# Kernel optimization log

Measured on AMD Instinct MI355X. Metric: run time of the kernel, lower is better.

Reference implementation:

```python
import jax, jax.numpy as jnp
import numpy as np

N_OBJ, N_EVT, N_EDGE, N_MAIN = 50000, 100000, 500000, 25000
OBJ_DIM, EVT_DIM = 256, 256


def setup_inputs() -> dict:
    key = jax.random.key(0)
    ks = jax.random.split(key, 12)
    s = 1.0 / np.sqrt(OBJ_DIM)
    return {
        "object_X": jax.random.normal(ks[0], (N_OBJ, OBJ_DIM), jnp.float32),
        "event_X": jax.random.normal(ks[1], (N_EVT, EVT_DIM), jnp.float32),
        "lc_obj_idx": jax.random.randint(ks[2], (N_EDGE,), 0, N_OBJ),
        "lc_evt_idx": jax.random.randint(ks[3], (N_EDGE,), 0, N_EVT),
        "main_idx": jax.random.randint(ks[4], (N_MAIN,), 0, N_OBJ),
        # lifecycle_proj: Linear(event_dim, obj_dim)
        "W_proj": jax.random.uniform(ks[5], (OBJ_DIM, EVT_DIM), jnp.float32, -s, s),
        "b_proj": jax.random.uniform(ks[6], (OBJ_DIM,), jnp.float32, -s, s),
        # GRUCell(obj_dim, obj_dim): weight_ih/hh are [3*H, H]
        "W_ih": jax.random.uniform(ks[7], (3 * OBJ_DIM, OBJ_DIM), jnp.float32, -s, s),
        "b_ih": jax.random.uniform(ks[8], (3 * OBJ_DIM,), jnp.float32, -s, s),
        "W_hh": jax.random.uniform(ks[9], (3 * OBJ_DIM, OBJ_DIM), jnp.float32, -s, s),
        "b_hh": jax.random.uniform(ks[10], (3 * OBJ_DIM,), jnp.float32, -s, s),
    }


def reference(object_X, event_X, lc_obj_idx, lc_evt_idx, main_idx,
              W_proj, b_proj, W_ih, b_ih, W_hh, b_hh):
    n_obj = object_X.shape[0]
    # gather event feats, linear + ReLU  -> [E, obj_dim]
    proj = jax.nn.relu(event_X[lc_evt_idx] @ W_proj.T + b_proj)
    # scatter_mean over target objects (empty slots -> 0, like torch_scatter)
    sums = jax.ops.segment_sum(proj, lc_obj_idx, num_segments=n_obj)
    cnt = jax.ops.segment_sum(jnp.ones((lc_obj_idx.shape[0],), proj.dtype),
                              lc_obj_idx, num_segments=n_obj)
    profile = sums / jnp.maximum(cnt, 1.0)[:, None]  # [N_obj, obj_dim]
    # GRUCell(profile, object_X)
    gi = profile @ W_ih.T + b_ih   # [N_obj, 3H]
    gh = object_X @ W_hh.T + b_hh  # [N_obj, 3H]
    i_r, i_z, i_n = jnp.split(gi, 3, axis=-1)
    h_r, h_z, h_n = jnp.split(gh, 3, axis=-1)
    r = jax.nn.sigmoid(i_r + h_r)
    z = jax.nn.sigmoid(i_z + h_z)
    n = jnp.tanh(i_n + r * h_n)
    updated = (1.0 - z) * n + z * object_X
    # masked blend: only main objects take updated values
    mask = jnp.zeros((n_obj, 1), object_X.dtype).at[main_idx].set(1.0)
    return mask * updated + (1.0 - mask) * object_X
```

## Files before the change

kernel.cpp:

```cpp
#include <hip/hip_runtime.h>

typedef unsigned short u16;
typedef __attribute__((ext_vector_type(8))) short bf16x8;
typedef __attribute__((ext_vector_type(4))) float f32x4;

struct __align__(8) u16x4_t { u16 x, y, z, w; };

__device__ __forceinline__ float b2f(u16 b) {
  union { unsigned u; float f; } v; v.u = ((unsigned)b) << 16; return v.f;
}
__device__ __forceinline__ u16 f2b(float f) {
  union { float f; unsigned u; } v; v.f = f;
  unsigned r = v.u + 0x7fffu + ((v.u >> 16) & 1u);
  return (u16)(r >> 16);
}

__global__ void set_mask_append(const int* __restrict__ main_idx, int* __restrict__ mask,
                                int* __restrict__ mlist, int* __restrict__ cpos,
                                int* __restrict__ mcount, int n) {
  int t = blockIdx.x * 256 + threadIdx.x;
  if (t >= n) return;
  int o = main_idx[t];
  if (atomicCAS(&mask[o], 0, 1) == 0) {
    int i = atomicAdd(mcount, 1);
    mlist[i] = o;
    cpos[o] = i;
  }
}

__global__ void cvt_weights(const float* __restrict__ Wp, const float* __restrict__ Wi,
                            const float* __restrict__ Wh, u16* __restrict__ wb) {
  int t = blockIdx.x * 256 + threadIdx.x;
  const float* src; int o;
  if (t < 16384)      { src = Wp; o = t; }
  else if (t < 65536) { src = Wi; o = t - 16384; }
  else                { src = Wh; o = t - 65536; }
  float4 v = ((const float4*)src)[o];
  u16x4_t q;
  q.x = f2b(v.x); q.y = f2b(v.y); q.z = f2b(v.z); q.w = f2b(v.w);
  ((u16x4_t*)wb)[t] = q;
}

__global__ void count_edges(const int* __restrict__ obj_idx, const int* __restrict__ mask,
                            int* __restrict__ deg, int n) {
  int e = blockIdx.x * 256 + threadIdx.x;
  if (e >= n) return;
  int o = obj_idx[e];
  if (mask[o]) atomicAdd(&deg[o], 1);
}

__global__ void scan_block(const int* __restrict__ deg, int* __restrict__ offs,
                           int* __restrict__ bsum, int n) {
  __shared__ int tmp[256];
  int t = threadIdx.x;
  int i = blockIdx.x * 256 + t;
  int v = (i < n) ? deg[i] : 0;
  tmp[t] = v;
  __syncthreads();
  for (int off = 1; off < 256; off <<= 1) {
    int x = (t >= off) ? tmp[t - off] : 0;
    __syncthreads();
    tmp[t] += x;
    __syncthreads();
  }
  if (i < n) offs[i] = tmp[t] - v;
  if (t == 255) bsum[blockIdx.x] = tmp[255];
}

__global__ void scan_tops(int* __restrict__ bsum, int nb) {
  __shared__ int tmp[256];
  int t = threadIdx.x;
  int v = (t < nb) ? bsum[t] : 0;
  tmp[t] = v;
  __syncthreads();
  for (int off = 1; off < 256; off <<= 1) {
    int x = (t >= off) ? tmp[t - off] : 0;
    __syncthreads();
    tmp[t] += x;
    __syncthreads();
  }
  if (t < nb) bsum[t] = tmp[t] - v;
}

__global__ void scan_add_rrows(int* __restrict__ offs, const int* __restrict__ bsum,
                               const int* __restrict__ mlist, const int* __restrict__ mcount,
                               int* __restrict__ rrows, int n, int Mpad) {
  int i = blockIdx.x * 256 + threadIdx.x;
  if (i < n) offs[i] += bsum[blockIdx.x];
  if (i < Mpad) {
    int mc = *mcount;
    rrows[i] = (i < mc) ? mlist[i] : 0;
  }
}

__global__ void fill_edges(const int* __restrict__ obj_idx, const int* __restrict__ evt_idx,
                           const int* __restrict__ mask, const int* __restrict__ offs,
                           int* __restrict__ cursor, int* __restrict__ elist, int n) {
  int e = blockIdx.x * 256 + threadIdx.x;
  if (e >= n) return;
  int o = obj_idx[e];
  if (!mask[o]) return;
  int pos = atomicAdd(&cursor[o], 1);
  elist[offs[o] + pos] = evt_idx[e];
}

__global__ __launch_bounds__(256)
void accum_prof(const u16* __restrict__ P, const int* __restrict__ elist,
                const int* __restrict__ offs, const int* __restrict__ deg,
                const int* __restrict__ mlist, const int* __restrict__ mcount,
                u16* __restrict__ prof, int Mpad) {
  const int wave = threadIdx.x >> 6;
  const int lane = threadIdx.x & 63;
  const int i = blockIdx.x * 4 + wave;
  if (i >= Mpad) return;
  const int mc = *mcount;
  float a0 = 0.f, a1 = 0.f, a2 = 0.f, a3 = 0.f;
  int d = 0;
  if (i < mc) {
    const int o = mlist[i];
    const int off = offs[o];
    d = deg[o];
    int j = 0;
    for (; j + 1 < d; j += 2) {
      int e0 = elist[off + j], e1 = elist[off + j + 1];
      u16x4_t p0 = *(const u16x4_t*)(P + (size_t)e0 * 256 + lane * 4);
      u16x4_t p1 = *(const u16x4_t*)(P + (size_t)e1 * 256 + lane * 4);
      a0 += b2f(p0.x) + b2f(p1.x);
      a1 += b2f(p0.y) + b2f(p1.y);
      a2 += b2f(p0.z) + b2f(p1.z);
      a3 += b2f(p0.w) + b2f(p1.w);
    }
    if (j < d) {
      int e0 = elist[off + j];
      u16x4_t p0 = *(const u16x4_t*)(P + (size_t)e0 * 256 + lane * 4);
      a0 += b2f(p0.x); a1 += b2f(p0.y); a2 += b2f(p0.z); a3 += b2f(p0.w);
    }
  }
  float s = 1.f / fmaxf((float)d, 1.f);
  u16x4_t ov;
  ov.x = f2b(a0 * s); ov.y = f2b(a1 * s); ov.z = f2b(a2 * s); ov.w = f2b(a3 * s);
  *(u16x4_t*)(prof + (size_t)i * 256 + lane * 4) = ov;
}

template<int RELU, int GATHER, int CVT>
__global__ __launch_bounds__(256, 2)
void gemm_bt(const u16* __restrict__ Ab, const float* __restrict__ Af,
             const u16* __restrict__ B, const float* __restrict__ bias,
             u16* __restrict__ C, const int* __restrict__ ridx,
             int M, int N, int K) {
  __shared__ u16 lA[128 * 64];
  __shared__ u16 lB[128 * 64];
  const int tid  = threadIdx.x;
  const int lane = tid & 63;
  const int wave = tid >> 6;
  const int m0 = blockIdx.x * 128;
  const int n0 = blockIdx.y * 128;

  f32x4 acc[4][4] = {};
  const int mR = (wave & 1) * 64;
  const int nC = (wave >> 1) * 64;

  int arow[4], brow[4], kkv[4];
#pragma unroll
  for (int s = 0; s < 4; ++s) {
    int slot = s * 256 + tid;
    int row  = slot >> 3;
    kkv[s]   = (slot & 7) * 8;
    int ar;
    if (GATHER) ar = ridx[m0 + row];
    else { ar = m0 + row; ar = (ar < M) ? ar : (M - 1); }
    arow[s] = ar;
    brow[s] = n0 + row;
  }

  for (int kt = 0; kt < K; kt += 64) {
    __syncthreads();
    float4 va[4][2];
#pragma unroll
    for (int s = 0; s < 4; ++s) {
      int slot = s * 256 + tid;
      const u16* gB = B + (size_t)brow[s] * K + (kt + kkv[s]);
      __builtin_amdgcn_global_load_lds(
          (const __attribute__((address_space(1))) void*)gB,
          (__attribute__((address_space(3))) void*)(lB + s * 2048 + wave * 512),
          16, 0, 0);
      if (CVT) {
        const float* gA = Af + (size_t)arow[s] * K + (kt + kkv[s]);
        va[s][0] = *(const float4*)gA;
        va[s][1] = *(const float4*)(gA + 4);
      } else {
        const u16* gA = Ab + (size_t)arow[s] * K + (kt + kkv[s]);
        __builtin_amdgcn_global_load_lds(
            (const __attribute__((address_space(1))) void*)gA,
            (__attribute__((address_space(3))) void*)(lA + s * 2048 + wave * 512),
            16, 0, 0);
      }
      (void)slot;
    }
    if (CVT) {
#pragma unroll
      for (int s = 0; s < 4; ++s) {
        int slot = s * 256 + tid;
        bf16x8 w;
        w[0] = (short)f2b(va[s][0].x); w[1] = (short)f2b(va[s][0].y);
        w[2] = (short)f2b(va[s][0].z); w[3] = (short)f2b(va[s][0].w);
        w[4] = (short)f2b(va[s][1].x); w[5] = (short)f2b(va[s][1].y);
        w[6] = (short)f2b(va[s][1].z); w[7] = (short)f2b(va[s][1].w);
        *(bf16x8*)(lA + slot * 8) = w;
      }
    }
    __syncthreads();

#pragma unroll
    for (int ks = 0; ks < 2; ++ks) {
      const int kb = ks * 32 + (lane >> 4) * 8;
      bf16x8 af[4], bfr[4];
#pragma unroll
      for (int i = 0; i < 4; ++i) {
        af[i]  = *(const bf16x8*)(lA + (mR + i * 16 + (lane & 15)) * 64 + kb);
        bfr[i] = *(const bf16x8*)(lB + (nC + i * 16 + (lane & 15)) * 64 + kb);
      }
#pragma unroll
      for (int i = 0; i < 4; ++i)
#pragma unroll
        for (int j = 0; j < 4; ++j)
          acc[i][j] = __builtin_amdgcn_mfma_f32_16x16x32_bf16(af[i], bfr[j], acc[i][j], 0, 0, 0);
    }
  }

  const int crow = (lane >> 4) * 4;
  const int ccol = lane & 15;
#pragma unroll
  for (int i = 0; i < 4; ++i) {
#pragma unroll
    for (int j = 0; j < 4; ++j) {
      int col = n0 + nC + j * 16 + ccol;
      float bv = bias[col];
#pragma unroll
      for (int q = 0; q < 4; ++q) {
        int row = m0 + mR + i * 16 + crow + q;
        if (row < M) {
          float v = acc[i][j][q] + bv;
          if (RELU) v = fmaxf(v, 0.f);
          C[(size_t)row * N + col] = f2b(v);
        }
      }
    }
  }
}

__global__ __launch_bounds__(256)
void gate_out(const u16* __restrict__ gi, const u16* __restrict__ gh,
              const float* __restrict__ objX, const int* __restrict__ mask,
              const int* __restrict__ cpos, float* __restrict__ out, int nObj) {
  const int row = blockIdx.x;
  const int d = threadIdx.x;
  const size_t o256 = (size_t)row * 256 + d;
  float x = objX[o256];
  float res = x;
  if (mask[row]) {
    const size_t c768 = (size_t)cpos[row] * 768 + d;
    float ir = b2f(gi[c768]), iz = b2f(gi[c768 + 256]), inn = b2f(gi[c768 + 512]);
    float hr = b2f(gh[c768]), hz = b2f(gh[c768 + 256]), hn = b2f(gh[c768 + 512]);
    float r = 1.f / (1.f + __expf(-(ir + hr)));
    float z = 1.f / (1.f + __expf(-(iz + hz)));
    float a = inn + r * hn;
    float n = 1.f - 2.f / (__expf(2.f * a) + 1.f);
    res = (1.f - z) * n + z * x;
  }
  out[o256] = res;
}


extern "C" void kernel_launch(void* const* d_in, const int* in_sizes, int n_in,
                              void* d_out, int out_size, void* d_ws, size_t ws_size,
                              hipStream_t stream) {
  const float* objX   = (const float*)d_in[0];
  const float* evtX   = (const float*)d_in[1];
  const int* obj_idx  = (const int*)d_in[2];
  const int* evt_idx  = (const int*)d_in[3];
  const int* main_idx = (const int*)d_in[4];
  const float* Wp = (const float*)d_in[5];
  const float* bp = (const float*)d_in[6];
  const float* Wi = (const float*)d_in[7];
  const float* bi = (const float*)d_in[8];
  const float* Wh = (const float*)d_in[9];
  const float* bh = (const float*)d_in[10];

  const int nObj  = in_sizes[0] / 256;
  const int nEvt  = in_sizes[1] / 256;
  const int nEdge = in_sizes[2];
  const int nMain = in_sizes[4];
  const int Mpad  = ((nMain + 127) / 128) * 128;

  char* ws = (char*)d_ws;
  u16*   P     = (u16*)(ws + 0);
  u16*   gi    = (u16*)(ws + 0);
  u16*   gh    = (u16*)(ws + 51200000);
  u16*   prof  = (u16*)(ws + 89735168);
  u16*   wb    = (u16*)(ws + 102580224);
  u16*   wpb   = wb;
  u16*   wib   = wb + 65536;
  u16*   whb   = wb + 262144;
  int*   deg   = (int*)(ws + 103497728);
  int*   offs  = (int*)(ws + 103697728);
  int*   cursor= (int*)(ws + 103897728);
  int*   mask  = (int*)(ws + 104097728);
  int*   cpos  = (int*)(ws + 104297728);
  int*   mlist = (int*)(ws + 104497728);
  int*   rrows = (int*)(ws + 104598080);
  int*   bsum  = (int*)(ws + 104698432);
  int*   mcount= (int*)(ws + 104699456);
  int*   elist = (int*)(ws + 104699520);
  float* out   = (float*)d_out;

  hipMemsetAsync(ws + 103497728, 0, 1201792, stream);

  set_mask_append<<<(nMain + 255) / 256, 256, 0, stream>>>(main_idx, mask, mlist, cpos, mcount, nMain);
  cvt_weights<<<448, 256, 0, stream>>>(Wp, Wi, Wh, wb);

  gemm_bt<1, 0, 1><<<dim3((nEvt + 127) / 128, 2), 256, 0, stream>>>(
      nullptr, evtX, wpb, bp, P, nullptr, nEvt, 256, 256);

  count_edges<<<(nEdge + 255) / 256, 256, 0, stream>>>(obj_idx, mask, deg, nEdge);
  scan_block<<<(nObj + 255) / 256, 256, 0, stream>>>(deg, offs, bsum, nObj);
  scan_tops<<<1, 256, 0, stream>>>(bsum, (nObj + 255) / 256);
  scan_add_rrows<<<(nObj + 255) / 256, 256, 0, stream>>>(offs, bsum, mlist, mcount, rrows, nObj, Mpad);
  fill_edges<<<(nEdge + 255) / 256, 256, 0, stream>>>(obj_idx, evt_idx, mask, offs, cursor, elist, nEdge);

  accum_prof<<<(Mpad + 3) / 4, 256, 0, stream>>>(P, elist, offs, deg, mlist, mcount, prof, Mpad);

  gemm_bt<0, 0, 0><<<dim3(Mpad / 128, 6), 256, 0, stream>>>(
      prof, nullptr, wib, bi, gi, nullptr, Mpad, 768, 256);
  gemm_bt<0, 1, 1><<<dim3(Mpad / 128, 6), 256, 0, stream>>>(
      nullptr, objX, whb, bh, gh, rrows, Mpad, 768, 256);

  gate_out<<<nObj, 256, 0, stream>>>(gi, gh, objX, mask, cpos, out, nObj);
}
```

Measured before the change: 422.8 us.

## Restructure GEMMs with resident swizzled B, replace global scan, fuse init kernels

The GEMM now loads the full 128x256 B tile into LDS once, with an XOR swizzle to avoid bank conflicts. A operands are read straight from global memory into registers, with a one-step prefetch and packed bf16 conversion, so the per-K-tile syncs go away. The three-kernel prefix scan over all objects is replaced by a wave-level scan over main objects only, with atomic allocation of offsets. Weight conversion and mask setup are fused into one launch, and gate_out is vectorised to one wave per row. The trade-offs are a larger LDS footprint (64KB per block), which may limit occupancy, and edge-list ordering that now depends on atomics.

Result: slower. 440.7 us (+4.2%).

```diff
diff --git a/kernel.cpp b/kernel.cpp
--- a/kernel.cpp
+++ b/kernel.cpp
@@ -14,31 +14,44 @@
   unsigned r = v.u + 0x7fffu + ((v.u >> 16) & 1u);
   return (u16)(r >> 16);
 }
-
-__global__ void set_mask_append(const int* __restrict__ main_idx, int* __restrict__ mask,
-                                int* __restrict__ mlist, int* __restrict__ cpos,
-                                int* __restrict__ mcount, int n) {
-  int t = blockIdx.x * 256 + threadIdx.x;
-  if (t >= n) return;
-  int o = main_idx[t];
-  if (atomicCAS(&mask[o], 0, 1) == 0) {
-    int i = atomicAdd(mcount, 1);
-    mlist[i] = o;
-    cpos[o] = i;
-  }
-}
-
-__global__ void cvt_weights(const float* __restrict__ Wp, const float* __restrict__ Wi,
-                            const float* __restrict__ Wh, u16* __restrict__ wb) {
-  int t = blockIdx.x * 256 + threadIdx.x;
-  const float* src; int o;
-  if (t < 16384)      { src = Wp; o = t; }
-  else if (t < 65536) { src = Wi; o = t - 16384; }
-  else                { src = Wh; o = t - 65536; }
-  float4 v = ((const float4*)src)[o];
-  u16x4_t q;
-  q.x = f2b(v.x); q.y = f2b(v.y); q.z = f2b(v.z); q.w = f2b(v.w);
-  ((u16x4_t*)wb)[t] = q;
+__device__ __forceinline__ unsigned pk2(float x, float y) {
+  union { float f; unsigned u; } a, b; a.f = x; b.f = y;
+  return __builtin_amdgcn_perm(b.u + 0x8000u, a.u + 0x8000u, 0x07060302u);
+}
+__device__ __forceinline__ bf16x8 pack8(float4 lo, float4 hi) {
+  union { bf16x8 v; unsigned u[4]; } t;
+  t.u[0] = pk2(lo.x, lo.y); t.u[1] = pk2(lo.z, lo.w);
+  t.u[2] = pk2(hi.x, hi.y); t.u[3] = pk2(hi.z, hi.w);
+  return t.v;
+}
+
+__global__ void init_misc(const float* __restrict__ Wp, const float* __restrict__ Wi,
+                          const float* __restrict__ Wh, u16* __restrict__ wb,
+                          const int* __restrict__ main_idx, int* __restrict__ mask,
+                          int* __restrict__ mlist, int* __restrict__ cpos,
+                          int* __restrict__ mcount, int nMain) {
+  int b = blockIdx.x;
+  if (b < 448) {
+    int t = b * 256 + threadIdx.x;
+    const float* src; int o;
+    if (t < 16384)      { src = Wp; o = t; }
+    else if (t < 65536) { src = Wi; o = t - 16384; }
+    else                { src = Wh; o = t - 65536; }
+    float4 v = ((const float4*)src)[o];
+    u16x4_t q;
+    q.x = f2b(v.x); q.y = f2b(v.y); q.z = f2b(v.z); q.w = f2b(v.w);
+    ((u16x4_t*)wb)[t] = q;
+  } else {
+    int t = (b - 448) * 256 + threadIdx.x;
+    if (t < nMain) {
+      int o = main_idx[t];
+      if (atomicCAS(&mask[o], 0, 1) == 0) {
+        int i = atomicAdd(mcount, 1);
+        mlist[i] = o;
+        cpos[o] = i;
+      }
+    }
+  }
 }
 
 __global__ void count_edges(const int* __restrict__ obj_idx, const int* __restrict__ mask,
@@ -49,48 +62,27 @@
   if (mask[o]) atomicAdd(&deg[o], 1);
 }
 
-__global__ void scan_block(const int* __restrict__ deg, int* __restrict__ offs,
-                           int* __restrict__ bsum, int n) {
-  __shared__ int tmp[256];
-  int t = threadIdx.x;
-  int i = blockIdx.x * 256 + t;
-  int v = (i < n) ? deg[i] : 0;
-  tmp[t] = v;
-  __syncthreads();
-  for (int off = 1; off < 256; off <<= 1) {
-    int x = (t >= off) ? tmp[t - off] : 0;
-    __syncthreads();
-    tmp[t] += x;
-    __syncthreads();
-  }
-  if (i < n) offs[i] = tmp[t] - v;
-  if (t == 255) bsum[blockIdx.x] = tmp[255];
-}
-
-__global__ void scan_tops(int* __restrict__ bsum, int nb) {
-  __shared__ int tmp[256];
-  int t = threadIdx.x;
-  int v = (t < nb) ? bsum[t] : 0;
-  tmp[t] = v;
-  __syncthreads();
-  for (int off = 1; off < 256; off <<= 1) {
-    int x = (t >= off) ? tmp[t - off] : 0;
-    __syncthreads();
-    tmp[t] += x;
-    __syncthreads();
-  }
-  if (t < nb) bsum[t] = tmp[t] - v;
-}
-
-__global__ void scan_add_rrows(int* __restrict__ offs, const int* __restrict__ bsum,
-                               const int* __restrict__ mlist, const int* __restrict__ mcount,
-                               int* __restrict__ rrows, int n, int Mpad) {
+__global__ __launch_bounds__(256)
+void alloc_offs(const int* __restrict__ mlist, const int* __restrict__ mcount,
+                const int* __restrict__ deg, int* __restrict__ offs,
+                int* __restrict__ tcur, int* __restrict__ rrows, int Mpad) {
   int i = blockIdx.x * 256 + threadIdx.x;
-  if (i < n) offs[i] += bsum[blockIdx.x];
-  if (i < Mpad) {
-    int mc = *mcount;
-    rrows[i] = (i < mc) ? mlist[i] : 0;
-  }
+  int lane = threadIdx.x & 63;
+  int mc = *mcount;
+  if (i < Mpad) rrows[i] = (i < mc) ? mlist[i] : 0;
+  int o = (i < mc) ? mlist[i] : 0;
+  int d = (i < mc) ? deg[o] : 0;
+  int x = d;
+#pragma unroll
+  for (int s = 1; s < 64; s <<= 1) {
+    int y = __shfl_up(x, s, 64);
+    if (lane >= s) x += y;
+  }
+  int wt = __shfl(x, 63, 64);
+  int base = 0;
+  if (lane == 63 && wt > 0) base = atomicAdd(tcur, wt);
+  base = __shfl(base, 63, 64);
+  if (i < mc) offs[o] = base + (x - d);
 }
 
 __global__ void fill_edges(const int* __restrict__ obj_idx, const int* __restrict__ evt_idx,
@@ -142,99 +134,104 @@
   *(u16x4_t*)(prof + (size_t)i * 256 + lane * 4) = ov;
 }
 
-template<int RELU, int GATHER, int CVT>
+template<int RELU, int GATHER, int AF32>
 __global__ __launch_bounds__(256, 2)
-void gemm_bt(const u16* __restrict__ Ab, const float* __restrict__ Af,
+void gemm_rs(const u16* __restrict__ Ab, const float* __restrict__ Af,
              const u16* __restrict__ B, const float* __restrict__ bias,
-             u16* __restrict__ C, const int* __restrict__ ridx,
-             int M, int N, int K) {
-  __shared__ u16 lA[128 * 64];
-  __shared__ u16 lB[128 * 64];
+             u16* __restrict__ C, const int* __restrict__ ridx, int M, int N) {
+  __shared__ u16 lB[128 * 256];
   const int tid  = threadIdx.x;
   const int lane = tid & 63;
   const int wave = tid >> 6;
   const int m0 = blockIdx.x * 128;
   const int n0 = blockIdx.y * 128;
-
-  f32x4 acc[4][4] = {};
   const int mR = (wave & 1) * 64;
   const int nC = (wave >> 1) * 64;
-
-  int arow[4], brow[4], kkv[4];
-#pragma unroll
-  for (int s = 0; s < 4; ++s) {
-    int slot = s * 256 + tid;
-    int row  = slot >> 3;
-    kkv[s]   = (slot & 7) * 8;
-    int ar;
-    if (GATHER) ar = ridx[m0 + row];
-    else { ar = m0 + row; ar = (ar < M) ? ar : (M - 1); }
-    arow[s] = ar;
-    brow[s] = n0 + row;
-  }
-
-  for (int kt = 0; kt < K; kt += 64) {
-    __syncthreads();
-    float4 va[4][2];
-#pragma unroll
-    for (int s = 0; s < 4; ++s) {
-      int slot = s * 256 + tid;
-      const u16* gB = B + (size_t)brow[s] * K + (kt + kkv[s]);
-      __builtin_amdgcn_global_load_lds(
-          (const __attribute__((address_space(1))) void*)gB,
-          (__attribute__((address_space(3))) void*)(lB + s * 2048 + wave * 512),
-          16, 0, 0);
-      if (CVT) {
-        const float* gA = Af + (size_t)arow[s] * K + (kt + kkv[s]);
-        va[s][0] = *(const float4*)gA;
-        va[s][1] = *(const float4*)(gA + 4);
-      } else {
-        const u16* gA = Ab + (size_t)arow[s] * K + (kt + kkv[s]);
-        __builtin_amdgcn_global_load_lds(
-            (const __attribute__((address_space(1))) void*)gA,
-            (__attribute__((address_space(3))) void*)(lA + s * 2048 + wave * 512),
-            16, 0, 0);
+  const int la15 = lane & 15;
+  const int kof  = (lane >> 4) * 8;
+
+  int arow[4];
+#pragma unroll
+  for (int i = 0; i < 4; ++i) {
+    int r = m0 + mR + i * 16 + la15;
+    if (GATHER) arow[i] = ridx[r];
+    else        arow[i] = (r < M) ? r : (M - 1);
+  }
+
+#pragma unroll
+  for (int s = 0; s < 16; ++s) {
+    int seg = s * 256 + tid;
+    int row = seg >> 5;
+    int cp  = seg & 31;
+    int c   = (cp & 24) | ((cp ^ row) & 7);
+    const u16* gB = B + (size_t)(n0 + row) * 256 + c * 8;
+    __builtin_amdgcn_global_load_lds(
+        (const __attribute__((address_space(1))) void*)gB,
+        (__attribute__((address_space(3))) void*)(lB + s * 2048 + wave * 512),
+        16, 0, 0);
+  }
+  __syncthreads();
+
+  f32x4 acc[4][4] = {};
+
+  const float* ap[4];
+  const u16*   abp[4];
+  float4 c0[4], c1[4];
+  if (AF32) {
+#pragma unroll
+    for (int i = 0; i < 4; ++i) {
+      ap[i] = Af + (size_t)arow[i] * 256 + kof;
+      c0[i] = *(const float4*)(ap[i]);
+      c1[i] = *(const float4*)(ap[i] + 4);
+    }
+  } else {
+#pragma unroll
+    for (int i = 0; i < 4; ++i) abp[i] = Ab + (size_t)arow[i] * 256 + kof;
+  }
+
+#pragma unroll
+  for (int ks = 0; ks < 8; ++ks) {
+    bf16x8 af[4], bfr[4];
+    if (AF32) {
+      float4 n0v[4], n1v[4];
+      if (ks < 7) {
+#pragma unroll
+        for (int i = 0; i < 4; ++i) {
+          n0v[i] = *(const float4*)(ap[i] + (ks + 1) * 32);
+          n1v[i] = *(const float4*)(ap[i] + (ks + 1) * 32 + 4);
+        }
       }
-      (void)slot;
-    }
-    if (CVT) {
-#pragma unroll
-      for (int s = 0; s < 4; ++s) {
-        int slot = s * 256 + tid;
-        bf16x8 w;
-        w[0] = (short)f2b(va[s][0].x); w[1] = (short)f2b(va[s][0].y);
-        w[2] = (short)f2b(va[s][0].z); w[3] = (short)f2b(va[s][0].w);
-        w[4] = (short)f2b(va[s][1].x); w[5] = (short)f2b(va[s][1].y);
-        w[6] = (short)f2b(va[s][1].z); w[7] = (short)f2b(va[s][1].w);
-        *(bf16x8*)(lA + slot * 8) = w;
+#pragma unroll
+      for (int i = 0; i < 4; ++i) af[i] = pack8(c0[i], c1[i]);
+      if (ks < 7) {
+#pragma unroll
+        for (int i = 0; i < 4; ++i) { c0[i] = n0v[i]; c1[i] = n1v[i]; }
       }
-    }
-    __syncthreads();
-
-#pragma unroll
-    for (int ks = 0; ks < 2; ++ks) {
-      const int kb = ks * 32 + (lane >> 4) * 8;
-      bf16x8 af[4], bfr[4];
-#pragma unroll
-      for (int i = 0; i < 4; ++i) {
-        af[i]  = *(const bf16x8*)(lA + (mR + i * 16 + (lane & 15)) * 64 + kb);
-        bfr[i] = *(const bf16x8*)(lB + (nC + i * 16 + (lane & 15)) * 64 + kb);
-      }
+    } else {
 #pragma unroll
       for (int i = 0; i < 4; ++i)
-#pragma unroll
-        for (int j = 0; j < 4; ++j)
-          acc[i][j] = __builtin_amdgcn_mfma_f32_16x16x32_bf16(af[i], bfr[j], acc[i][j], 0, 0, 0);
-    }
+        af[i] = *(const bf16x8*)(abp[i] + ks * 32);
+    }
+#pragma unroll
+    for (int j = 0; j < 4; ++j) {
+      int rj = nC + j * 16 + la15;
+      int c  = ks * 4 + (lane >> 4);
+      int cp = (c & 24) | ((c ^ rj) & 7);
+      bfr[j] = *(const bf16x8*)(lB + rj * 256 + cp * 8);
+    }
+#pragma unroll
+    for (int i = 0; i < 4; ++i)
+#pragma unroll
+      for (int j = 0; j < 4; ++j)
+        acc[i][j] = __builtin_amdgcn_mfma_f32_16x16x32_bf16(af[i], bfr[j], acc[i][j], 0, 0, 0);
   }
 
   const int crow = (lane >> 4) * 4;
-  const int ccol = lane & 15;
 #pragma unroll
   for (int i = 0; i < 4; ++i) {
 #pragma unroll
     for (int j = 0; j < 4; ++j) {
-      int col = n0 + nC + j * 16 + ccol;
+      int col = n0 + nC + j * 16 + la15;
       float bv = bias[col];
 #pragma unroll
       for (int q = 0; q < 4; ++q) {
@@ -253,22 +250,39 @@
 void gate_out(const u16* __restrict__ gi, const u16* __restrict__ gh,
               const float* __restrict__ objX, const int* __restrict__ mask,
               const int* __restrict__ cpos, float* __restrict__ out, int nObj) {
-  const int row = blockIdx.x;
-  const int d = threadIdx.x;
-  const size_t o256 = (size_t)row * 256 + d;
-  float x = objX[o256];
-  float res = x;
+  const int wave = threadIdx.x >> 6;
+  const int lane = threadIdx.x & 63;
+  const int row = blockIdx.x * 4 + wave;
+  if (row >= nObj) return;
+  float4 x4 = *(const float4*)(objX + (size_t)row * 256 + lane * 4);
+  float4 r4 = x4;
   if (mask[row]) {
-    const size_t c768 = (size_t)cpos[row] * 768 + d;
-    float ir = b2f(gi[c768]), iz = b2f(gi[c768 + 256]), inn = b2f(gi[c768 + 512]);
-    float hr = b2f(gh[c768]), hz = b2f(gh[c768 + 256]), hn = b2f(gh[c768 + 512]);
-    float r = 1.f / (1.f + __expf(-(ir + hr)));
-    float z = 1.f / (1.f + __expf(-(iz + hz)));
-    float a = inn + r * hn;
-    float n = 1.f - 2.f / (__expf(2.f * a) + 1.f);
-    res = (1.f - z) * n + z * x;
-  }
-  out[o256] = res;
+    size_t b = (size_t)cpos[row] * 768 + lane * 4;
+    u16x4_t ir = *(const u16x4_t*)(gi + b);
+    u16x4_t iz = *(const u16x4_t*)(gi + b + 256);
+    u16x4_t in_ = *(const u16x4_t*)(gi + b + 512);
+    u16x4_t hr = *(const u16x4_t*)(gh + b);
+    u16x4_t hz = *(const u16x4_t*)(gh + b + 256);
+    u16x4_t hn = *(const u16x4_t*)(gh + b + 512);
+    float xs[4] = {x4.x, x4.y, x4.z, x4.w};
+    u16 irs[4] = {ir.x, ir.y, ir.z, ir.w};
+    u16 izs[4] = {iz.x, iz.y, iz.z, iz.w};
+    u16 ins[4] = {in_.x, in_.y, in_.z, in_.w};
+    u16 hrs[4] = {hr.x, hr.y, hr.z, hr.w};
+    u16 hzs[4] = {hz.x, hz.y, hz.z, hz.w};
+    u16 hns[4] = {hn.x, hn.y, hn.z, hn.w};
+    float rs[4];
+#pragma unroll
+    for (int q = 0; q < 4; ++q) {
+      float r = 1.f / (1.f + __expf(-(b2f(irs[q]) + b2f(hrs[q]))));
+      float z = 1.f / (1.f + __expf(-(b2f(izs[q]) + b2f(hzs[q]))));
+      float a = b2f(ins[q]) + r * b2f(hns[q]);
+      float n = 1.f - 2.f / (__expf(2.f * a) + 1.f);
+      rs[q] = (1.f - z) * n + z * xs[q];
+    }
+    r4.x = rs[0]; r4.y = rs[1]; r4.z = rs[2]; r4.w = rs[3];
+  }
+  *(float4*)(out + (size_t)row * 256 + lane * 4) = r4;
 }
 
 
@@ -303,37 +317,34 @@
   u16*   wib   = wb + 65536;
   u16*   whb   = wb + 262144;
   int*   deg   = (int*)(ws + 103497728);
-  int*   offs  = (int*)(ws + 103697728);
-  int*   cursor= (int*)(ws + 103897728);
-  int*   mask  = (int*)(ws + 104097728);
-  int*   cpos  = (int*)(ws + 104297728);
-  int*   mlist = (int*)(ws + 104497728);
-  int*   rrows = (int*)(ws + 104598080);
-  int*   bsum  = (int*)(ws + 104698432);
-  int*   mcount= (int*)(ws + 104699456);
-  int*   elist = (int*)(ws + 104699520);
+  int*   cursor= (int*)(ws + 103697728);
+  int*   mask  = (int*)(ws + 103897728);
+  int*   mcount= (int*)(ws + 104097728);
+  int*   tcur  = (int*)(ws + 104097792);
+  int*   cpos  = (int*)(ws + 104097856);
+  int*   offs  = (int*)(ws + 104297856);
+  int*   mlist = (int*)(ws + 104497856);
+  int*   rrows = (int*)(ws + 104598208);
+  int*   elist = (int*)(ws + 104698560);
   float* out   = (float*)d_out;
 
-  hipMemsetAsync(ws + 103497728, 0, 1201792, stream);
-
-  set_mask_append<<<(nMain + 255) / 256, 256, 0, stream>>>(main_idx, mask, mlist, cpos, mcount, nMain);
-  cvt_weights<<<448, 256, 0, stream>>>(Wp, Wi, Wh, wb);
-
-  gemm_bt<1, 0, 1><<<dim3((nEvt + 127) / 128, 2), 256, 0, stream>>>(
-      nullptr, evtX, wpb, bp, P, nullptr, nEvt, 256, 256);
+  hipMemsetAsync(ws + 103497728, 0, 600128, stream);
+
+  init_misc<<<546, 256, 0, stream>>>(Wp, Wi, Wh, wb, main_idx, mask, mlist, cpos, mcount, nMain);
+
+  gemm_rs<1, 0, 1><<<dim3((nEvt + 127) / 128, 2), 256, 0, stream>>>(
+      nullptr, evtX, wpb, bp, P, nullptr, nEvt, 256);
 
   count_edges<<<(nEdge + 255) / 256, 256, 0, stream>>>(obj_idx, mask, deg, nEdge);
-  scan_block<<<(nObj + 255) / 256, 256, 0, stream>>>(deg, offs, bsum, nObj);
-  scan_tops<<<1, 256, 0, stream>>>(bsum, (nObj + 255) / 256);
-  scan_add_rrows<<<(nObj + 255) / 256, 256, 0, stream>>>(offs, bsum, mlist, mcount, rrows, nObj, Mpad);
+  alloc_offs<<<Mpad / 256, 256, 0, stream>>>(mlist, mcount, deg, offs, tcur, rrows, Mpad);
   fill_edges<<<(nEdge + 255) / 256, 256, 0, stream>>>(obj_idx, evt_idx, mask, offs, cursor, elist, nEdge);
 
   accum_prof<<<(Mpad + 3) / 4, 256, 0, stream>>>(P, elist, offs, deg, mlist, mcount, prof, Mpad);
 
-  gemm_bt<0, 0, 0><<<dim3(Mpad / 128, 6), 256, 0, stream>>>(
-      prof, nullptr, wib, bi, gi, nullptr, Mpad, 768, 256);
-  gemm_bt<0, 1, 1><<<dim3(Mpad / 128, 6), 256, 0, stream>>>(
-      nullptr, objX, whb, bh, gh, rrows, Mpad, 768, 256);
-
-  gate_out<<<nObj, 256, 0, stream>>>(gi, gh, objX, mask, cpos, out, nObj);
-}
+  gemm_rs<0, 0, 0><<<dim3(Mpad / 128, 6), 256, 0, stream>>>(
+      prof, nullptr, wib, bi, gi, nullptr, Mpad, 768);
+  gemm_rs<0, 1, 1><<<dim3(Mpad / 128, 6), 256, 0, stream>>>(
+      nullptr, objX, whb, bh, gh, rrows, Mpad, 768);
+
+  gate_out<<<(nObj + 3) / 4, 256, 0, stream>>>(gi, gh, objX, mask, cpos, out, nObj);
+}
```
